# Performance work log

Measured on AMD Instinct MI355X. Metric: run time of the kernel, lower is better.

The kernel has to match this reference:

```python
import jax, jax.numpy as jnp
import numpy as np

T, B = 64, 32
POS_V, WORD_V = 48, 32000
P_EMB, W_EMB = 128, 512
P_HID, W_HID = 256, 1024


def setup_inputs() -> dict:
    key = jax.random.key(0)
    ks = iter(jax.random.split(key, 40))
    def prm(shape, s=0.05):
        return jax.random.normal(next(ks), shape, dtype=jnp.float32) * s
    z = lambda *shape: jnp.zeros(shape, jnp.float32)
    inp = {
        'pos': jax.random.randint(next(ks), (T, B), 0, POS_V),
        'word': jax.random.randint(next(ks), (T, B), 0, WORD_V),
        'pos_emb_W': prm((POS_V, P_EMB)),
        'word_emb_W': prm((WORD_V, W_EMB)),
        'w2p_W': prm((W_HID, W_HID)), 'w2p_b': z(W_HID),
        'p2w_W': prm((P_HID, P_HID)), 'p2w_b': z(P_HID),
        'p_Wih0': prm((4 * P_HID, P_EMB + W_HID)), 'p_Whh0': prm((4 * P_HID, P_HID)),
        'p_bih0': z(4 * P_HID), 'p_bhh0': z(4 * P_HID),
        'w_Wih0': prm((4 * W_HID, W_EMB + P_HID)), 'w_Whh0': prm((4 * W_HID, W_HID)),
        'w_bih0': z(4 * W_HID), 'w_bhh0': z(4 * W_HID),
        'w_Wih1': prm((4 * W_HID, W_HID)), 'w_Whh1': prm((4 * W_HID, W_HID)),
        'w_bih1': z(4 * W_HID), 'w_bhh1': z(4 * W_HID),
        'pos_proj_W': prm((POS_V, P_HID)), 'pos_proj_b': z(POS_V),
        'word_proj1_W': prm((W_EMB, W_HID)), 'word_proj1_b': z(W_EMB),
        'word_proj2_b': z(WORD_V),
    }
    return inp


def _lstm_cell(x, h, c, Wih, Whh, bih, bhh):
    # PyTorch LSTMCell: gates ordered i, f, g, o
    g = x @ Wih.T + h @ Whh.T + bih + bhh
    i, f, gg, o = jnp.split(g, 4, axis=-1)
    c_new = jax.nn.sigmoid(f) * c + jax.nn.sigmoid(i) * jnp.tanh(gg)
    h_new = jax.nn.sigmoid(o) * jnp.tanh(c_new)
    return h_new, c_new


def reference(pos, word, pos_emb_W, word_emb_W, w2p_W, w2p_b, p2w_W, p2w_b,
              p_Wih0, p_Whh0, p_bih0, p_bhh0,
              w_Wih0, w_Whh0, w_bih0, w_bhh0,
              w_Wih1, w_Whh1, w_bih1, w_bhh1,
              pos_proj_W, pos_proj_b, word_proj1_W, word_proj1_b, word_proj2_b):
    p_emb = pos_emb_W[pos]    # [T, B, P_EMB]
    w_emb = word_emb_W[word]  # [T, B, W_EMB]
    Bn = pos.shape[1]
    p_layers = [(p_Wih0, p_Whh0, p_bih0, p_bhh0)]
    w_layers = [(w_Wih0, w_Whh0, w_bih0, w_bhh0), (w_Wih1, w_Whh1, w_bih1, w_bhh1)]
    ph = p_Whh0.shape[1]
    wh = w_Whh0.shape[1]
    init = (jnp.zeros((1, Bn, ph), jnp.float32), jnp.zeros((1, Bn, ph), jnp.float32),
            jnp.zeros((2, Bn, wh), jnp.float32), jnp.zeros((2, Bn, wh), jnp.float32))

    def step(carry, xs):
        p_h, p_c, w_h, w_c = carry
        p_t, w_t = xs
        # word_gate on word-RNN last hidden at t-1, conditions POS-RNN at t
        last_w = jnp.tanh(w_h[-1] @ w2p_W.T + w2p_b)
        x = jnp.concatenate([p_t, last_w], axis=-1)
        new_ph, new_pc = [], []
        for li, (Wih, Whh, bih, bhh) in enumerate(p_layers):
            h, c = _lstm_cell(x, p_h[li], p_c[li], Wih, Whh, bih, bhh)
            new_ph.append(h); new_pc.append(c); x = h
        p_out = jax.nn.log_softmax(x @ pos_proj_W.T + pos_proj_b, axis=-1)
        # pos_gate on POS-RNN last hidden at t, conditions word-RNN at t
        last_p = jnp.tanh(new_ph[-1] @ p2w_W.T + p2w_b)
        x = jnp.concatenate([w_t, last_p], axis=-1)
        new_wh, new_wc = [], []
        for li, (Wih, Whh, bih, bhh) in enumerate(w_layers):
            h, c = _lstm_cell(x, w_h[li], w_c[li], Wih, Whh, bih, bhh)
            new_wh.append(h); new_wc.append(c); x = h
        # tied word projection: hid -> emb -> vocab with embedding weight
        w_logits = (x @ word_proj1_W.T + word_proj1_b) @ word_emb_W.T + word_proj2_b
        w_out = jax.nn.log_softmax(w_logits, axis=-1)
        carry = (jnp.stack(new_ph), jnp.stack(new_pc), jnp.stack(new_wh), jnp.stack(new_wc))
        return carry, (p_out, w_out)

    _, (p_outs, w_outs) = jax.lax.scan(step, init, (p_emb, w_emb))
    return p_outs, w_outs
```

## Files before the change

kernel.cpp:

```cpp
#include <hip/hip_runtime.h>
#include <math.h>

#define LSTR 36

__device__ __forceinline__ void gemm_core(
    const float* __restrict__ A, int lda,
    const float* __restrict__ W, int ldw,
    int n0, int N, int K,
    const float* __restrict__ b1, const float* __restrict__ b2,
    int act, float* __restrict__ C, int ldc, int row0,
    float* As, float* Ws)
{
    const int tid = threadIdx.x;
    const int jl = tid & 15;
    const int bg = tid >> 4;
    float acc[4][4] = {{0.f,0.f,0.f,0.f},{0.f,0.f,0.f,0.f},{0.f,0.f,0.f,0.f},{0.f,0.f,0.f,0.f}};

    float4 ra[2], rw[4];

    int ar[2], akv[2], wr[4], wkv[4];
#pragma unroll
    for (int p = 0; p < 2; ++p) {
        int i = tid + 128 * p;
        ar[p] = i >> 3; akv[p] = (i & 7) << 2;
    }
#pragma unroll
    for (int p = 0; p < 4; ++p) {
        int i = tid + 128 * p;
        wr[p] = i >> 3; wkv[p] = (i & 7) << 2;
    }

#pragma unroll
    for (int p = 0; p < 2; ++p)
        ra[p] = *(const float4*)(A + (size_t)(row0 + ar[p]) * lda + akv[p]);
#pragma unroll
    for (int p = 0; p < 4; ++p) {
        int n = n0 + wr[p];
        rw[p] = (n < N) ? *(const float4*)(W + (size_t)n * ldw + wkv[p])
                        : make_float4(0.f, 0.f, 0.f, 0.f);
    }

    for (int kk = 0; kk < K; kk += 32) {
#pragma unroll
        for (int p = 0; p < 2; ++p)
            *(float4*)&As[ar[p] * LSTR + akv[p]] = ra[p];
#pragma unroll
        for (int p = 0; p < 4; ++p)
            *(float4*)&Ws[wr[p] * LSTR + wkv[p]] = rw[p];
        __syncthreads();

        if (kk + 32 < K) {
            int kn = kk + 32;
#pragma unroll
            for (int p = 0; p < 2; ++p)
                ra[p] = *(const float4*)(A + (size_t)(row0 + ar[p]) * lda + kn + akv[p]);
#pragma unroll
            for (int p = 0; p < 4; ++p) {
                int n = n0 + wr[p];
                rw[p] = (n < N) ? *(const float4*)(W + (size_t)n * ldw + kn + wkv[p])
                                : make_float4(0.f, 0.f, 0.f, 0.f);
            }
        }

#pragma unroll
        for (int k4 = 0; k4 < 8; ++k4) {
            float4 av[4], wv[4];
#pragma unroll
            for (int jb = 0; jb < 4; ++jb) av[jb] = *(float4*)&As[(bg + 8 * jb) * LSTR + k4 * 4];
#pragma unroll
            for (int jn = 0; jn < 4; ++jn) wv[jn] = *(float4*)&Ws[(jl + 16 * jn) * LSTR + k4 * 4];
#pragma unroll
            for (int jn = 0; jn < 4; ++jn)
#pragma unroll
                for (int jb = 0; jb < 4; ++jb) {
                    acc[jn][jb] += av[jb].x * wv[jn].x;
                    acc[jn][jb] += av[jb].y * wv[jn].y;
                    acc[jn][jb] += av[jb].z * wv[jn].z;
                    acc[jn][jb] += av[jb].w * wv[jn].w;
                }
        }
        __syncthreads();
    }

#pragma unroll
    for (int jn = 0; jn < 4; ++jn) {
        int n = n0 + jl + 16 * jn;
        if (n < N) {
            float bb = (b1 ? b1[n] : 0.f) + (b2 ? b2[n] : 0.f);
#pragma unroll
            for (int jb = 0; jb < 4; ++jb) {
                int b = bg + 8 * jb;
                float x = acc[jn][jb] + bb;
                if (act == 1) x = tanhf(x);
                C[(size_t)(row0 + b) * ldc + n] = x;
            }
        }
    }
}

__global__ void __launch_bounds__(128) gemm_generic(
    const float* __restrict__ A, int lda, const float* __restrict__ W, int ldw,
    const float* __restrict__ b1, const float* __restrict__ b2,
    float* __restrict__ C, int ldc, int N, int K, int act, int swapxy)
{
    __shared__ __align__(16) float As[32 * LSTR];
    __shared__ __align__(16) float Ws[64 * LSTR];
    int bn = swapxy ? blockIdx.y : blockIdx.x;
    int bm = swapxy ? blockIdx.x : blockIdx.y;
    gemm_core(A, lda, W, ldw, bn * 64, N, K, b1, b2, act, C, ldc, bm * 32, As, Ws);
}

__global__ void __launch_bounds__(128) step_pre(
    int t, const float* __restrict__ Hw1, const float* __restrict__ Hp,
    const float* __restrict__ h_w0,
    const float* __restrict__ w2p_W, const float* __restrict__ w2p_b,
    const float* __restrict__ p_Whh0,
    const float* __restrict__ w_Whh0, const float* __restrict__ w_Whh1,
    const float* __restrict__ w_bih1, const float* __restrict__ w_bhh1,
    float* __restrict__ u, float* __restrict__ hp_hh,
    float* __restrict__ w0_hh, float* __restrict__ w1_hh)
{
    __shared__ __align__(16) float As[32 * LSTR];
    __shared__ __align__(16) float Ws[64 * LSTR];
    int blk = blockIdx.x;
    const float* hw1 = Hw1 + (size_t)t * 32 * 1024;
    const float* hp  = Hp  + (size_t)t * 32 * 256;
    if (blk < 16)
        gemm_core(hw1, 1024, w2p_W, 1024, blk * 64, 1024, 1024, w2p_b, nullptr, 1, u, 1024, 0, As, Ws);
    else if (blk < 32)
        gemm_core(hp, 256, p_Whh0, 256, (blk - 16) * 64, 1024, 256, nullptr, nullptr, 0, hp_hh, 1024, 0, As, Ws);
    else if (blk < 96)
        gemm_core(h_w0, 1024, w_Whh0, 1024, (blk - 32) * 64, 4096, 1024, nullptr, nullptr, 0, w0_hh, 4096, 0, As, Ws);
    else
        gemm_core(hw1, 1024, w_Whh1, 1024, (blk - 96) * 64, 4096, 1024, w_bih1, w_bhh1, 0, w1_hh, 4096, 0, As, Ws);
}

__global__ void __launch_bounds__(128) lstm_cell(
    const float* __restrict__ A, int K,
    const float* __restrict__ Wih, int ldw, int H,
    const float* __restrict__ addA, int ldA,
    const float* __restrict__ addB, int ldB,
    float* __restrict__ h_out, float* __restrict__ c_state)
{
    __shared__ __align__(16) float As[32 * LSTR];
    __shared__ __align__(16) float Ws[64 * LSTR];
    const int tid = threadIdx.x;
    const int jl = tid & 15;
    const int bg = tid >> 4;
    const int j0 = blockIdx.x * 16;
    float acc[4][4] = {{0.f,0.f,0.f,0.f},{0.f,0.f,0.f,0.f},{0.f,0.f,0.f,0.f},{0.f,0.f,0.f,0.f}};

    float4 ra[2], rw[4];
    int ar[2], akv[2], wr[4], wkv[4], wrow[4];
#pragma unroll
    for (int p = 0; p < 2; ++p) {
        int i = tid + 128 * p;
        ar[p] = i >> 3; akv[p] = (i & 7) << 2;
    }
#pragma unroll
    for (int p = 0; p < 4; ++p) {
        int i = tid + 128 * p;
        wr[p] = i >> 3; wkv[p] = (i & 7) << 2;
        wrow[p] = (wr[p] >> 4) * H + j0 + (wr[p] & 15);
    }

#pragma unroll
    for (int p = 0; p < 2; ++p)
        ra[p] = *(const float4*)(A + (size_t)ar[p] * K + akv[p]);
#pragma unroll
    for (int p = 0; p < 4; ++p)
        rw[p] = *(const float4*)(Wih + (size_t)wrow[p] * ldw + wkv[p]);

    for (int kk = 0; kk < K; kk += 32) {
#pragma unroll
        for (int p = 0; p < 2; ++p)
            *(float4*)&As[ar[p] * LSTR + akv[p]] = ra[p];
#pragma unroll
        for (int p = 0; p < 4; ++p)
            *(float4*)&Ws[wr[p] * LSTR + wkv[p]] = rw[p];
        __syncthreads();

        if (kk + 32 < K) {
            int kn = kk + 32;
#pragma unroll
            for (int p = 0; p < 2; ++p)
                ra[p] = *(const float4*)(A + (size_t)ar[p] * K + kn + akv[p]);
#pragma unroll
            for (int p = 0; p < 4; ++p)
                rw[p] = *(const float4*)(Wih + (size_t)wrow[p] * ldw + kn + wkv[p]);
        }

#pragma unroll
        for (int k4 = 0; k4 < 8; ++k4) {
            float4 av[4], wv[4];
#pragma unroll
            for (int jb = 0; jb < 4; ++jb) av[jb] = *(float4*)&As[(bg + 8 * jb) * LSTR + k4 * 4];
#pragma unroll
            for (int jn = 0; jn < 4; ++jn) wv[jn] = *(float4*)&Ws[(jl + 16 * jn) * LSTR + k4 * 4];
#pragma unroll
            for (int jn = 0; jn < 4; ++jn)
#pragma unroll
                for (int jb = 0; jb < 4; ++jb) {
                    acc[jn][jb] += av[jb].x * wv[jn].x;
                    acc[jn][jb] += av[jb].y * wv[jn].y;
                    acc[jn][jb] += av[jb].z * wv[jn].z;
                    acc[jn][jb] += av[jb].w * wv[jn].w;
                }
        }
        __syncthreads();
    }

    const int j = j0 + jl;
#pragma unroll
    for (int jb = 0; jb < 4; ++jb) {
        int b = bg + 8 * jb;
        float g[4];
#pragma unroll
        for (int jn = 0; jn < 4; ++jn) {
            int row = jn * H + j;
            float x = acc[jn][jb];
            if (addA) x += addA[(size_t)b * ldA + row];
            if (addB) x += addB[(size_t)b * ldB + row];
            g[jn] = x;
        }
        float c_old = c_state[b * H + j];
        float ii = 1.f / (1.f + expf(-g[0]));
        float ff = 1.f / (1.f + expf(-g[1]));
        float gg = tanhf(g[2]);
        float oo = 1.f / (1.f + expf(-g[3]));
        float cn = ff * c_old + ii * gg;
        float hn = oo * tanhf(cn);
        c_state[b * H + j] = cn;
        h_out[b * H + j] = hn;
    }
}

__global__ void __launch_bounds__(128) gather_emb(
    const int* __restrict__ pos, const int* __restrict__ word,
    const float* __restrict__ pe, const float* __restrict__ we,
    float* __restrict__ Xp, float* __restrict__ Xw)
{
    int row = blockIdx.x;
    int p = pos[row];
    int w = word[row];
    for (int i = threadIdx.x; i < 128; i += 128)
        Xp[(size_t)row * 128 + i] = pe[(size_t)p * 128 + i];
    for (int i = threadIdx.x; i < 512; i += 128)
        Xw[(size_t)row * 512 + i] = we[(size_t)w * 512 + i];
}

__global__ void __launch_bounds__(256) pos_out_k(
    const float* __restrict__ Hp, const float* __restrict__ W,
    const float* __restrict__ bias, float* __restrict__ out)
{
    int row = blockIdx.x * 4 + (threadIdx.x >> 6);
    int lane = threadIdx.x & 63;
    const float* h = Hp + (size_t)row * 256;
    float logit = -INFINITY;
    if (lane < 48) {
        float s = bias[lane];
        const float* w = W + (size_t)lane * 256;
        for (int k = 0; k < 256; k += 4) {
            s += h[k] * w[k];
            s += h[k + 1] * w[k + 1];
            s += h[k + 2] * w[k + 2];
            s += h[k + 3] * w[k + 3];
        }
        logit = s;
    }
    float m = logit;
    for (int off = 1; off < 64; off <<= 1) m = fmaxf(m, __shfl_xor(m, off));
    float e = (lane < 48) ? expf(logit - m) : 0.f;
    float ssum = e;
    for (int off = 1; off < 64; off <<= 1) ssum += __shfl_xor(ssum, off);
    float ls = m + logf(ssum);
    if (lane < 48) out[(size_t)row * 48 + lane] = logit - ls;
}

__global__ void __launch_bounds__(256) logsoftmax_w(float* __restrict__ out)
{
    __shared__ float redm[256], reds[256];
    int row = blockIdx.x;
    float* p = out + (size_t)row * 32000;
    float4* p4 = (float4*)p;
    int tid = threadIdx.x;

    float m = -INFINITY, s = 0.f;
    for (int i = tid; i < 8000; i += 256) {
        float4 v = p4[i];
        float x;
        x = v.x; if (x > m) { s = s * expf(m - x) + 1.f; m = x; } else s += expf(x - m);
        x = v.y; if (x > m) { s = s * expf(m - x) + 1.f; m = x; } else s += expf(x - m);
        x = v.z; if (x > m) { s = s * expf(m - x) + 1.f; m = x; } else s += expf(x - m);
        x = v.w; if (x > m) { s = s * expf(m - x) + 1.f; m = x; } else s += expf(x - m);
    }
    redm[tid] = m; reds[tid] = s;
    __syncthreads();
    for (int st = 128; st > 0; st >>= 1) {
        if (tid < st) {
            float m2 = redm[tid + st], s2 = reds[tid + st];
            float M = fmaxf(redm[tid], m2);
            reds[tid] = reds[tid] * expf(redm[tid] - M) + s2 * expf(m2 - M);
            redm[tid] = M;
        }
        __syncthreads();
    }
    float ls = redm[0] + logf(reds[0]);

    for (int i = tid; i < 8000; i += 256) {
        float4 v = p4[i];
        v.x -= ls; v.y -= ls; v.z -= ls; v.w -= ls;
        p4[i] = v;
    }
}

extern "C" void kernel_launch(void* const* d_in, const int* in_sizes, int n_in,
                              void* d_out, int out_size, void* d_ws, size_t ws_size,
                              hipStream_t stream)
{
    const int T = 64, B = 32, TB = T * B;

    const int*   pos         = (const int*)d_in[0];
    const int*   word        = (const int*)d_in[1];
    const float* pos_emb_W   = (const float*)d_in[2];
    const float* word_emb_W  = (const float*)d_in[3];
    const float* w2p_W       = (const float*)d_in[4];
    const float* w2p_b       = (const float*)d_in[5];
    const float* p2w_W       = (const float*)d_in[6];
    const float* p2w_b       = (const float*)d_in[7];
    const float* p_Wih0      = (const float*)d_in[8];
    const float* p_Whh0      = (const float*)d_in[9];
    const float* p_bih0      = (const float*)d_in[10];
    const float* p_bhh0      = (const float*)d_in[11];
    const float* w_Wih0      = (const float*)d_in[12];
    const float* w_Whh0      = (const float*)d_in[13];
    const float* w_bih0      = (const float*)d_in[14];
    const float* w_bhh0      = (const float*)d_in[15];
    const float* w_Wih1      = (const float*)d_in[16];
    const float* w_Whh1      = (const float*)d_in[17];
    const float* w_bih1      = (const float*)d_in[18];
    const float* w_bhh1      = (const float*)d_in[19];
    const float* pos_proj_W  = (const float*)d_in[20];
    const float* pos_proj_b  = (const float*)d_in[21];
    const float* word_proj1W = (const float*)d_in[22];
    const float* word_proj1b = (const float*)d_in[23];
    const float* word_proj2b = (const float*)d_in[24];

    float* out   = (float*)d_out;
    float* Pout  = out;
    float* Wout  = out + (size_t)TB * 48;

    float* ws = (float*)d_ws;
    size_t off = 0;
    auto alloc = [&](size_t n) { float* p = ws + off; off += n; return p; };
    float* Xp    = alloc((size_t)TB * 128);
    float* Xw    = alloc((size_t)TB * 512);
    float* Ap    = alloc((size_t)TB * 1024);
    float* Hp    = alloc((size_t)(TB + B) * 256);
    float* Hw1   = alloc((size_t)(TB + B) * 1024);
    float* E     = alloc((size_t)TB * 512);
    float* c_p   = alloc((size_t)B * 256);
    float* h_w0  = alloc((size_t)B * 1024);
    float* c_w0  = alloc((size_t)B * 1024);
    float* c_w1  = alloc((size_t)B * 1024);
    float* u     = alloc((size_t)B * 1024);
    float* v     = alloc((size_t)B * 256);
    float* hp_hh = alloc((size_t)B * 1024);
    float* w0_hh = alloc((size_t)B * 4096);
    float* w1_hh = alloc((size_t)B * 4096);

    float* Aw = Wout;

    hipMemsetAsync(c_p, 0, (size_t)(B * 256 + 3 * B * 1024) * 4, stream);
    hipMemsetAsync(Hp,  0, (size_t)B * 256 * 4, stream);
    hipMemsetAsync(Hw1, 0, (size_t)B * 1024 * 4, stream);

    gather_emb<<<TB, 128, 0, stream>>>(pos, word, pos_emb_W, word_emb_W, Xp, Xw);
    gemm_generic<<<dim3(16, 64), 128, 0, stream>>>(Xp, 128, p_Wih0, 1152,
        p_bih0, p_bhh0, Ap, 1024, 1024, 128, 0, 0);
    gemm_generic<<<dim3(64, 64), 128, 0, stream>>>(Xw, 512, w_Wih0, 768,
        w_bih0, w_bhh0, Aw, 4096, 4096, 512, 0, 0);

    for (int t = 0; t < T; ++t) {
        step_pre<<<160, 128, 0, stream>>>(t, Hw1, Hp, h_w0,
            w2p_W, w2p_b, p_Whh0, w_Whh0, w_Whh1, w_bih1, w_bhh1,
            u, hp_hh, w0_hh, w1_hh);
        lstm_cell<<<16, 128, 0, stream>>>(u, 1024, p_Wih0 + 128, 1152, 256,
            Ap + (size_t)t * 32 * 1024, 1024, hp_hh, 1024,
            Hp + (size_t)(t + 1) * 32 * 256, c_p);
        gemm_generic<<<dim3(4, 1), 128, 0, stream>>>(
            Hp + (size_t)(t + 1) * 32 * 256, 256, p2w_W, 256,
            p2w_b, nullptr, v, 256, 256, 256, 1, 0);
        lstm_cell<<<64, 128, 0, stream>>>(v, 256, w_Wih0 + 512, 768, 1024,
            Aw + (size_t)t * 32 * 4096, 4096, w0_hh, 4096, h_w0, c_w0);
        lstm_cell<<<64, 128, 0, stream>>>(h_w0, 1024, w_Wih1, 1024, 1024,
            nullptr, 0, w1_hh, 4096,
            Hw1 + (size_t)(t + 1) * 32 * 1024, c_w1);
    }

    gemm_generic<<<dim3(8, 64), 128, 0, stream>>>(Hw1 + 32 * 1024, 1024,
        word_proj1W, 1024, word_proj1b, nullptr, E, 512, 512, 1024, 0, 0);
    gemm_generic<<<dim3(64, 500), 128, 0, stream>>>(E, 512, word_emb_W, 512,
        word_proj2b, nullptr, Wout, 32000, 32000, 512, 0, 1);
    logsoftmax_w<<<TB, 256, 0, stream>>>(Wout);
    pos_out_k<<<TB / 4, 256, 0, stream>>>(Hp + 32 * 256, pos_proj_W, pos_proj_b, Pout);
}
```

Baseline: 27.00 ms.

## Fuse the recurrent time loop into one persistent kernel with grid barriers

Replaces the 320 per-step kernel launches (step_pre plus four LSTM/gate kernels per timestep) with a single persistent kernel of 160 blocks. The stages are separated by atomic-counter grid barriers, with one counter slot per barrier. This targets launch overhead and inter-kernel gaps on the serial recurrence. It assumes all 160 blocks are co-resident, otherwise the barriers deadlock. Many blocks also sit idle during the small stages.

```diff
diff --git a/kernel.cpp b/kernel.cpp
--- a/kernel.cpp
+++ b/kernel.cpp
@@ -2,6 +2,21 @@
 #include <math.h>
 
 #define LSTR 36
+
+__device__ __forceinline__ void gbar(unsigned* cnts, int idx, unsigned nb)
+{
+    __syncthreads();
+    if (threadIdx.x == 0) {
+        __threadfence();
+        __hip_atomic_fetch_add(&cnts[idx], 1u, __ATOMIC_ACQ_REL,
+                               __HIP_MEMORY_SCOPE_AGENT);
+        while (__hip_atomic_load(&cnts[idx], __ATOMIC_RELAXED,
+                                 __HIP_MEMORY_SCOPE_AGENT) < nb)
+            __builtin_amdgcn_s_sleep(2);
+        __threadfence();
+    }
+    __syncthreads();
+}
 
 __device__ __forceinline__ void gemm_core(
     const float* __restrict__ A, int lda,
@@ -17,7 +32,6 @@
     float acc[4][4] = {{0.f,0.f,0.f,0.f},{0.f,0.f,0.f,0.f},{0.f,0.f,0.f,0.f},{0.f,0.f,0.f,0.f}};
 
     float4 ra[2], rw[4];
-
     int ar[2], akv[2], wr[4], wkv[4];
 #pragma unroll
     for (int p = 0; p < 2; ++p) {
@@ -110,44 +124,18 @@
     gemm_core(A, lda, W, ldw, bn * 64, N, K, b1, b2, act, C, ldc, bm * 32, As, Ws);
 }
 
-__global__ void __launch_bounds__(128) step_pre(
-    int t, const float* __restrict__ Hw1, const float* __restrict__ Hp,
-    const float* __restrict__ h_w0,
-    const float* __restrict__ w2p_W, const float* __restrict__ w2p_b,
-    const float* __restrict__ p_Whh0,
-    const float* __restrict__ w_Whh0, const float* __restrict__ w_Whh1,
-    const float* __restrict__ w_bih1, const float* __restrict__ w_bhh1,
-    float* __restrict__ u, float* __restrict__ hp_hh,
-    float* __restrict__ w0_hh, float* __restrict__ w1_hh)
-{
-    __shared__ __align__(16) float As[32 * LSTR];
-    __shared__ __align__(16) float Ws[64 * LSTR];
-    int blk = blockIdx.x;
-    const float* hw1 = Hw1 + (size_t)t * 32 * 1024;
-    const float* hp  = Hp  + (size_t)t * 32 * 256;
-    if (blk < 16)
-        gemm_core(hw1, 1024, w2p_W, 1024, blk * 64, 1024, 1024, w2p_b, nullptr, 1, u, 1024, 0, As, Ws);
-    else if (blk < 32)
-        gemm_core(hp, 256, p_Whh0, 256, (blk - 16) * 64, 1024, 256, nullptr, nullptr, 0, hp_hh, 1024, 0, As, Ws);
-    else if (blk < 96)
-        gemm_core(h_w0, 1024, w_Whh0, 1024, (blk - 32) * 64, 4096, 1024, nullptr, nullptr, 0, w0_hh, 4096, 0, As, Ws);
-    else
-        gemm_core(hw1, 1024, w_Whh1, 1024, (blk - 96) * 64, 4096, 1024, w_bih1, w_bhh1, 0, w1_hh, 4096, 0, As, Ws);
-}
-
-__global__ void __launch_bounds__(128) lstm_cell(
+__device__ __forceinline__ void lstm_core(
     const float* __restrict__ A, int K,
     const float* __restrict__ Wih, int ldw, int H,
     const float* __restrict__ addA, int ldA,
     const float* __restrict__ addB, int ldB,
-    float* __restrict__ h_out, float* __restrict__ c_state)
-{
-    __shared__ __align__(16) float As[32 * LSTR];
-    __shared__ __align__(16) float Ws[64 * LSTR];
+    float* __restrict__ h_out, float* __restrict__ c_state,
+    int blk, float* As, float* Ws)
+{
     const int tid = threadIdx.x;
     const int jl = tid & 15;
     const int bg = tid >> 4;
-    const int j0 = blockIdx.x * 16;
+    const int j0 = blk * 16;
     float acc[4][4] = {{0.f,0.f,0.f,0.f},{0.f,0.f,0.f,0.f},{0.f,0.f,0.f,0.f},{0.f,0.f,0.f,0.f}};
 
     float4 ra[2], rw[4];
@@ -232,6 +220,67 @@
         float hn = oo * tanhf(cn);
         c_state[b * H + j] = cn;
         h_out[b * H + j] = hn;
+    }
+}
+
+struct RecArgs {
+    const float *w2p_W, *w2p_b, *p_Whh0;
+    const float *w_Whh0, *w_Whh1, *w_bih1, *w_bhh1;
+    const float *p_Wih0, *p2w_W, *p2w_b, *w_Wih0, *w_Wih1;
+    const float *Ap, *Aw;
+    float *u, *hp_hh, *w0_hh, *w1_hh, *v;
+    float *Hp, *Hw1, *h_w0, *c_p, *c_w0, *c_w1;
+    unsigned *bar;
+};
+
+__global__ void __launch_bounds__(128) recurrence(RecArgs a)
+{
+    __shared__ __align__(16) float As[32 * LSTR];
+    __shared__ __align__(16) float Ws[64 * LSTR];
+    const int blk = blockIdx.x;
+    const unsigned nb = gridDim.x;
+    int bi = 0;
+
+    for (int t = 0; t < 64; ++t) {
+        const float* hw1 = a.Hw1 + (size_t)t * 32 * 1024;
+        const float* hp  = a.Hp  + (size_t)t * 32 * 256;
+
+        if (blk < 16)
+            gemm_core(hw1, 1024, a.w2p_W, 1024, blk * 64, 1024, 1024,
+                      a.w2p_b, nullptr, 1, a.u, 1024, 0, As, Ws);
+        else if (blk < 32)
+            gemm_core(hp, 256, a.p_Whh0, 256, (blk - 16) * 64, 1024, 256,
+                      nullptr, nullptr, 0, a.hp_hh, 1024, 0, As, Ws);
+        else if (blk < 96)
+            gemm_core(a.h_w0, 1024, a.w_Whh0, 1024, (blk - 32) * 64, 4096, 1024,
+                      nullptr, nullptr, 0, a.w0_hh, 4096, 0, As, Ws);
+        else
+            gemm_core(hw1, 1024, a.w_Whh1, 1024, (blk - 96) * 64, 4096, 1024,
+                      a.w_bih1, a.w_bhh1, 0, a.w1_hh, 4096, 0, As, Ws);
+        gbar(a.bar, bi++, nb);
+
+        if (blk < 16)
+            lstm_core(a.u, 1024, a.p_Wih0 + 128, 1152, 256,
+                      a.Ap + (size_t)t * 32 * 1024, 1024, a.hp_hh, 1024,
+                      a.Hp + (size_t)(t + 1) * 32 * 256, a.c_p, blk, As, Ws);
+        gbar(a.bar, bi++, nb);
+
+        if (blk < 4)
+            gemm_core(a.Hp + (size_t)(t + 1) * 32 * 256, 256, a.p2w_W, 256,
+                      blk * 64, 256, 256, a.p2w_b, nullptr, 1, a.v, 256, 0, As, Ws);
+        gbar(a.bar, bi++, nb);
+
+        if (blk < 64)
+            lstm_core(a.v, 256, a.w_Wih0 + 512, 768, 1024,
+                      a.Aw + (size_t)t * 32 * 4096, 4096, a.w0_hh, 4096,
+                      a.h_w0, a.c_w0, blk, As, Ws);
+        gbar(a.bar, bi++, nb);
+
+        if (blk < 64)
+            lstm_core(a.h_w0, 1024, a.w_Wih1, 1024, 1024,
+                      nullptr, 0, a.w1_hh, 4096,
+                      a.Hw1 + (size_t)(t + 1) * 32 * 1024, a.c_w1, blk, As, Ws);
+        gbar(a.bar, bi++, nb);
     }
 }
 
@@ -368,12 +417,14 @@
     float* hp_hh = alloc((size_t)B * 1024);
     float* w0_hh = alloc((size_t)B * 4096);
     float* w1_hh = alloc((size_t)B * 4096);
+    unsigned* bar = (unsigned*)alloc(512);
 
     float* Aw = Wout;
 
     hipMemsetAsync(c_p, 0, (size_t)(B * 256 + 3 * B * 1024) * 4, stream);
     hipMemsetAsync(Hp,  0, (size_t)B * 256 * 4, stream);
     hipMemsetAsync(Hw1, 0, (size_t)B * 1024 * 4, stream);
+    hipMemsetAsync(bar, 0, 512 * 4, stream);
 
     gather_emb<<<TB, 128, 0, stream>>>(pos, word, pos_emb_W, word_emb_W, Xp, Xw);
     gemm_generic<<<dim3(16, 64), 128, 0, stream>>>(Xp, 128, p_Wih0, 1152,
@@ -381,22 +432,17 @@
     gemm_generic<<<dim3(64, 64), 128, 0, stream>>>(Xw, 512, w_Wih0, 768,
         w_bih0, w_bhh0, Aw, 4096, 4096, 512, 0, 0);
 
-    for (int t = 0; t < T; ++t) {
-        step_pre<<<160, 128, 0, stream>>>(t, Hw1, Hp, h_w0,
-            w2p_W, w2p_b, p_Whh0, w_Whh0, w_Whh1, w_bih1, w_bhh1,
-            u, hp_hh, w0_hh, w1_hh);
-        lstm_cell<<<16, 128, 0, stream>>>(u, 1024, p_Wih0 + 128, 1152, 256,
-            Ap + (size_t)t * 32 * 1024, 1024, hp_hh, 1024,
-            Hp + (size_t)(t + 1) * 32 * 256, c_p);
-        gemm_generic<<<dim3(4, 1), 128, 0, stream>>>(
-            Hp + (size_t)(t + 1) * 32 * 256, 256, p2w_W, 256,
-            p2w_b, nullptr, v, 256, 256, 256, 1, 0);
-        lstm_cell<<<64, 128, 0, stream>>>(v, 256, w_Wih0 + 512, 768, 1024,
-            Aw + (size_t)t * 32 * 4096, 4096, w0_hh, 4096, h_w0, c_w0);
-        lstm_cell<<<64, 128, 0, stream>>>(h_w0, 1024, w_Wih1, 1024, 1024,
-            nullptr, 0, w1_hh, 4096,
-            Hw1 + (size_t)(t + 1) * 32 * 1024, c_w1);
-    }
+    RecArgs ra;
+    ra.w2p_W = w2p_W; ra.w2p_b = w2p_b; ra.p_Whh0 = p_Whh0;
+    ra.w_Whh0 = w_Whh0; ra.w_Whh1 = w_Whh1; ra.w_bih1 = w_bih1; ra.w_bhh1 = w_bhh1;
+    ra.p_Wih0 = p_Wih0; ra.p2w_W = p2w_W; ra.p2w_b = p2w_b;
+    ra.w_Wih0 = w_Wih0; ra.w_Wih1 = w_Wih1;
+    ra.Ap = Ap; ra.Aw = Aw;
+    ra.u = u; ra.hp_hh = hp_hh; ra.w0_hh = w0_hh; ra.w1_hh = w1_hh; ra.v = v;
+    ra.Hp = Hp; ra.Hw1 = Hw1; ra.h_w0 = h_w0;
+    ra.c_p = c_p; ra.c_w0 = c_w0; ra.c_w1 = c_w1;
+    ra.bar = bar;
+    recurrence<<<160, 128, 0, stream>>>(ra);
 
     gemm_generic<<<dim3(8, 64), 128, 0, stream>>>(Hw1 + 32 * 1024, 1024,
         word_proj1W, 1024, word_proj1b, nullptr, E, 512, 512, 1024, 0, 0);
```

After: 30.00 ms. 1.11x slower.
